# Optimization experiments

Measured on AMD Instinct MI355X. Metric: run time of the kernel, lower is better.

The kernel has to match this reference:

```python
import jax, jax.numpy as jnp
import numpy as np

B, S, D, H, HD, NF, NL, V = 16, 2048, 768, 12, 64, 32, 12, 2362
EPS = 1e-6  # fast_transformers LinearAttention eps


def _rope_tables(seq_len, dim):
    inv_freq = 1.0 / (10000.0 ** (jnp.arange(0, dim, 2, dtype=jnp.float32) / dim))
    t = jnp.arange(seq_len, dtype=jnp.float32)
    freqs = jnp.einsum('s,f->sf', t, inv_freq)
    emb = jnp.concatenate([freqs, freqs], axis=-1)[None, :, None, :]  # [1,S,1,HD]
    return jnp.cos(emb), jnp.sin(emb)


def _rot_half(x):
    x1, x2 = jnp.split(x, 2, axis=-1)
    return jnp.concatenate([-x2, x1], axis=-1)


def _ln(x, g, b):
    m = jnp.mean(x, axis=-1, keepdims=True)
    v = jnp.var(x, axis=-1, keepdims=True)
    return (x - m) / jnp.sqrt(v + 1e-5) * g + b


def setup_inputs():
    key = jax.random.key(0)
    ks = jax.random.split(key, 16)
    w = lambda k, shape: jax.random.normal(k, shape, jnp.float32) * 0.02
    return {
        'idx': jax.random.randint(ks[0], (B, S), 0, V),
        'mask': jnp.ones((B, S), jnp.int32),
        'emb': w(ks[1], (V, D)),
        'wq': w(ks[2], (NL, D, D)), 'bq': jnp.zeros((NL, D), jnp.float32),
        'wk': w(ks[3], (NL, D, D)), 'bk': jnp.zeros((NL, D), jnp.float32),
        'wv': w(ks[4], (NL, D, D)), 'bv': jnp.zeros((NL, D), jnp.float32),
        'wo': w(ks[5], (NL, D, D)), 'bo': jnp.zeros((NL, D), jnp.float32),
        'omega': jax.random.normal(ks[6], (NL, HD, NF), jnp.float32),
        'g1': jnp.ones((NL, D), jnp.float32), 'be1': jnp.zeros((NL, D), jnp.float32),
        'w1': w(ks[7], (NL, D, D)), 'c1': jnp.zeros((NL, D), jnp.float32),
        'w2': w(ks[8], (NL, D, D)), 'c2': jnp.zeros((NL, D), jnp.float32),
        'g2': jnp.ones((NL, D), jnp.float32), 'be2': jnp.zeros((NL, D), jnp.float32),
        'gf': jnp.ones((D,), jnp.float32), 'bf': jnp.zeros((D,), jnp.float32),
    }


def reference(idx, mask, emb, wq, bq, wk, bk, wv, bv, wo, bo, omega,
              g1, be1, w1, c1, w2, c2, g2, be2, gf, bf):
    x = emb[idx]                     # token embedding [B,S,D]; dropout = identity (eval)
    m = mask.astype(x.dtype)         # LengthMask from mask.sum(-1); mask is contiguous ones
    cos, sin = _rope_tables(S, HD)
    for l in range(NL):
        q = (x @ wq[l] + bq[l]).reshape(B, S, H, HD)
        k = (x @ wk[l] + bk[l]).reshape(B, S, H, HD)
        v = (x @ wv[l] + bv[l]).reshape(B, S, H, HD)
        q = q * cos + _rot_half(q) * sin
        k = k * cos + _rot_half(k) * sin
        # GeneralizedRandomFeatures: phi(x) = relu(x @ omega)
        Qf = jax.nn.relu(jnp.einsum('bshd,df->bshf', q, omega[l]))
        Kf = jax.nn.relu(jnp.einsum('bshd,df->bshf', k, omega[l])) * m[:, :, None, None]
        KV = jnp.einsum('bshf,bshd->bhfd', Kf, v)                       # [B,H,NF,HD]
        Z = 1.0 / (jnp.einsum('bshf,bhf->bsh', Qf, Kf.sum(axis=1)) + EPS)
        a = jnp.einsum('bshf,bhfd,bsh->bshd', Qf, KV, Z).reshape(B, S, D)
        x = x + (a @ wo[l] + bo[l])           # residual (dropout=identity)
        x = _ln(x, g1[l], be1[l])             # post-norm
        y = jax.nn.gelu(x @ w1[l] + c1[l], approximate=False) @ w2[l] + c2[l]
        x = _ln(x + y, g2[l], be2[l])
    return _ln(x, gf, bf)                     # final encoder LayerNorm
```

## Files before the change

kernel.cpp:

```cpp
#include <hip/hip_runtime.h>
#include <cstdint>
#include <cstddef>

typedef __bf16 bf16;
typedef __bf16 bf16x8 __attribute__((ext_vector_type(8)));
typedef __bf16 bf16x4 __attribute__((ext_vector_type(4)));
typedef float f32x4 __attribute__((ext_vector_type(4)));

#define NB 16
#define SS 2048
#define HH 12
#define NLL 12
#define MTOK (NB*SS)

#define BARRIER() do { asm volatile("" ::: "memory"); __builtin_amdgcn_s_barrier(); asm volatile("" ::: "memory"); } while (0)
#define VMCNT0()  asm volatile("s_waitcnt vmcnt(0)" ::: "memory")
#define SCHEDB()  __builtin_amdgcn_sched_barrier(0)

__device__ __forceinline__ void load16_lds(const bf16* g, bf16* l) {
    __builtin_amdgcn_global_load_lds((const __attribute__((address_space(1))) void*)g,
                                     (__attribute__((address_space(3))) void*)l, 16, 0, 0);
}

__global__ void diag_k(float* out, float code) {
    if (threadIdx.x == 0 && blockIdx.x == 0) out[0] = code;
}

__global__ __launch_bounds__(256) void packw_k(const float* __restrict__ wq, const float* __restrict__ wk,
                                               const float* __restrict__ wv, const float* __restrict__ wo,
                                               const float* __restrict__ w1, const float* __restrict__ w2,
                                               int l, bf16* qkvT_l, bf16* oT_l, bf16* w1T_l, bf16* w2T_l) {
    __shared__ float tile[32][33];
    int which = blockIdx.z;
    const float* srcs[6] = {wq, wk, wv, wo, w1, w2};
    const float* src = srcs[which] + (size_t)l * 589824;
    bf16* dst;
    if (which < 3)       dst = qkvT_l + (size_t)which * 589824;
    else if (which == 3) dst = oT_l;
    else if (which == 4) dst = w1T_l;
    else                 dst = w2T_l;
    int tx = threadIdx.x, ty = threadIdx.y;
    int bx = blockIdx.x, by = blockIdx.y;
#pragma unroll
    for (int j = 0; j < 4; ++j)
        tile[ty + j*8][tx] = src[(size_t)(by*32 + ty + j*8) * 768 + bx*32 + tx];
    __syncthreads();
#pragma unroll
    for (int j = 0; j < 4; ++j)
        dst[(size_t)(bx*32 + ty + j*8) * 768 + by*32 + tx] = (bf16)tile[tx][ty + j*8];
}

__global__ void packb_k(const float* __restrict__ bq, const float* __restrict__ bk,
                        const float* __restrict__ bv, float* bqkv) {
    int i = blockIdx.x * 256 + threadIdx.x;
    if (i >= NLL * 2304) return;
    int l = i / 2304, c = i % 2304;
    float v = (c < 768) ? bq[l*768 + c] : (c < 1536) ? bk[l*768 + c - 768] : bv[l*768 + c - 1536];
    bqkv[i] = v;
}

__global__ void rope_k(float* cosT, float* sinT) {
    int i = blockIdx.x * 256 + threadIdx.x;
    int s = i >> 6, j = i & 63, f = j & 31;
    float inv = powf(10000.f, -(float)(2*f) * (1.0f/64.0f));
    float ang = (float)s * inv;
    cosT[i] = cosf(ang);
    sinT[i] = sinf(ang);
}

__global__ __launch_bounds__(192) void embed_k(const int* __restrict__ idx, const float* __restrict__ emb,
                                               float* __restrict__ x, bf16* __restrict__ xb) {
    size_t tok = blockIdx.x;
    int t = threadIdx.x;
    int id = idx[tok];
    float4 v = *(const float4*)&emb[(size_t)id * 768 + t*4];
    *(float4*)&x[tok * 768 + t*4] = v;
    bf16x4 o; o[0] = (bf16)v.x; o[1] = (bf16)v.y; o[2] = (bf16)v.z; o[3] = (bf16)v.w;
    *(bf16x4*)&xb[tok * 768 + t*4] = o;
}

__global__ __launch_bounds__(512, 2)
void gemm256_k(const bf16* __restrict__ A, const bf16* __restrict__ Bt,
               const float* __restrict__ bias, bf16* __restrict__ outb, int N) {
    const int K = 768;
    __shared__ bf16 As[2][16384];
    __shared__ bf16 Bs[2][16384];
    const int t = threadIdx.x;
    const int w = t >> 6, lane = t & 63;
    const int wr = w >> 2, wc = w & 3;

    const int nx = gridDim.x;
    const int L = blockIdx.y * nx + blockIdx.x;
    const int xcd = L & 7, bi = L >> 3;
    const int bcol = (bi % nx) * 256;
    const int brow = ((bi / nx) * 8 + xcd) * 256;

    const int srow0 = t >> 3;
    const int scb   = (t & 7) * 16;
    const int scbs  = scb ^ ((srow0 & 7) << 4);
    const int scol  = scbs >> 1;

    auto stageA = [&](int s, int k0, int hh) {
        const bf16* g0 = A + (size_t)(brow + hh*128 + srow0)      * K + k0 + scol;
        const bf16* g1 = A + (size_t)(brow + hh*128 + srow0 + 64) * K + k0 + scol;
        load16_lds(g0, &As[s][hh*8192 + t*8]);
        load16_lds(g1, &As[s][hh*8192 + t*8 + 4096]);
    };
    auto stageB = [&](int s, int k0, int hh) {
        const bf16* g0 = Bt + (size_t)(bcol + hh*128 + srow0)      * K + k0 + scol;
        const bf16* g1 = Bt + (size_t)(bcol + hh*128 + srow0 + 64) * K + k0 + scol;
        load16_lds(g0, &Bs[s][hh*8192 + t*8]);
        load16_lds(g1, &Bs[s][hh*8192 + t*8 + 4096]);
    };

    const int rowa = lane & 15, kg = lane >> 4;
    const int rsw  = (rowa & 7) << 4;

    f32x4  acc[8][4] = {};
    bf16x8 af[4][2];
    bf16x8 bg[2][2][2];

#define LOADAF(CUR, MH)                                                          \
    _Pragma("unroll") for (int mi2 = 0; mi2 < 4; ++mi2)                          \
    _Pragma("unroll") for (int ks = 0; ks < 2; ++ks) {                           \
        int lrow = wr*128 + (MH)*64 + mi2*16 + rowa;                             \
        int cbyt = (ks*64 + kg*16) ^ rsw;                                        \
        af[mi2][ks] = *(const bf16x8*)&As[CUR][lrow*64 + (cbyt >> 1)];           \
    }
#define LOADBG(CUR, NH)                                                          \
    _Pragma("unroll") for (int ni2 = 0; ni2 < 2; ++ni2)                          \
    _Pragma("unroll") for (int ks = 0; ks < 2; ++ks) {                           \
        int lrow = wc*64 + (NH)*32 + ni2*16 + rowa;                              \
        int cbyt = (ks*64 + kg*16) ^ rsw;                                        \
        bg[NH][ni2][ks] = *(const bf16x8*)&Bs[CUR][lrow*64 + (cbyt >> 1)];       \
    }
#define MFMAQ(MH, NH)                                                            \
    __builtin_amdgcn_s_setprio(1);                                               \
    _Pragma("unroll") for (int mi2 = 0; mi2 < 4; ++mi2)                          \
    _Pragma("unroll") for (int ni2 = 0; ni2 < 2; ++ni2)                          \
    _Pragma("unroll") for (int ks = 0; ks < 2; ++ks)                             \
        acc[(MH)*4+mi2][(NH)*2+ni2] = __builtin_amdgcn_mfma_f32_16x16x32_bf16(   \
            af[mi2][ks], bg[NH][ni2][ks], acc[(MH)*4+mi2][(NH)*2+ni2], 0, 0, 0); \
    __builtin_amdgcn_s_setprio(0);

    stageA(0, 0, 0); stageA(0, 0, 1); stageB(0, 0, 0); stageB(0, 0, 1);
    VMCNT0();
    BARRIER();

    for (int kt = 0; kt < 12; ++kt) {
        const int cur = kt & 1, nb = cur ^ 1;
        const int kn = (kt + 1) * 64;
        const bool st = (kt < 11);
        if (st) { stageA(nb, kn, 0); stageA(nb, kn, 1); stageB(nb, kn, 0); stageB(nb, kn, 1); }
        LOADAF(cur, 0);
        LOADBG(cur, 0);
        MFMAQ(0, 0);
        SCHEDB();
        LOADBG(cur, 1);
        MFMAQ(0, 1);
        SCHEDB();
        LOADAF(cur, 1);
        MFMAQ(1, 1);
        SCHEDB();
        MFMAQ(1, 0);
        VMCNT0();
        BARRIER();
    }
#undef LOADAF
#undef LOADBG
#undef MFMAQ

    bf16* Cs = &As[0][0];
    const int r0 = (lane >> 4) * 4, c0 = lane & 15;
    const int ch = t & 15, rr = t >> 4;
#pragma unroll
    for (int h = 0; h < 2; ++h) {
        __syncthreads();
        if ((wc >> 1) == h) {
            const int lc0 = (wc & 1) * 64;
#pragma unroll
            for (int mi = 0; mi < 8; ++mi)
#pragma unroll
                for (int ni = 0; ni < 4; ++ni) {
                    int col = bcol + wc * 64 + ni * 16 + c0;
                    float bv = bias[col];
#pragma unroll
                    for (int r = 0; r < 4; ++r)
                        Cs[(wr*128 + mi*16 + r0 + r) * 128 + lc0 + ni*16 + c0] =
                            (bf16)(acc[mi][ni][r] + bv);
                }
        }
        __syncthreads();
#pragma unroll
        for (int i = 0; i < 8; ++i) {
            int row = rr + i * 32;
            *(bf16x8*)&outb[(size_t)(brow + row) * N + bcol + h*128 + ch*8] =
                *(const bf16x8*)&Cs[row * 128 + ch * 8];
        }
    }
}

template <int MODE>
__global__ __launch_bounds__(256)
void gemm128_k(const bf16* __restrict__ A, const bf16* __restrict__ Bt,
               const float* __restrict__ bias, bf16* __restrict__ outb, int N) {
    const int K = 768;
    __shared__ bf16 sh[16384];
    bf16* As = sh;
    bf16* Bs = sh + 8192;
    const int t = threadIdx.x;
    const int w = t >> 6, lane = t & 63;
    const int wr = w >> 1, wc = w & 1;

    const int nx = gridDim.x;
    const int L = blockIdx.y * nx + blockIdx.x;
    const int xcd = L & 7, bi = L >> 3;
    const int bcol = (bi % nx) * 128;
    const int brow = ((bi / nx) * 8 + xcd) * 128;

    const int srow = t >> 3;
    const int scol = (((t & 7) * 16) ^ ((srow & 7) << 4)) >> 1;
    const int rowa = lane & 15, kg = lane >> 4;
    const int rsw  = (rowa & 7) << 4;

    f32x4 acc[4][4] = {};

    for (int k0 = 0; k0 < K; k0 += 64) {
        __syncthreads();
#pragma unroll
        for (int j = 0; j < 4; ++j) {
            load16_lds(A  + (size_t)(brow + j*32 + srow) * K + k0 + scol, &As[j*2048 + t*8]);
            load16_lds(Bt + (size_t)(bcol + j*32 + srow) * K + k0 + scol, &Bs[j*2048 + t*8]);
        }
        __syncthreads();
        bf16x8 af[4][2], bg[4][2];
#pragma unroll
        for (int mi = 0; mi < 4; ++mi)
#pragma unroll
            for (int ks = 0; ks < 2; ++ks)
                af[mi][ks] = *(const bf16x8*)&As[(wr*64 + mi*16 + rowa)*64 + (((ks*64 + kg*16) ^ rsw) >> 1)];
#pragma unroll
        for (int ni = 0; ni < 4; ++ni)
#pragma unroll
            for (int ks = 0; ks < 2; ++ks)
                bg[ni][ks] = *(const bf16x8*)&Bs[(wc*64 + ni*16 + rowa)*64 + (((ks*64 + kg*16) ^ rsw) >> 1)];
#pragma unroll
        for (int mi = 0; mi < 4; ++mi)
#pragma unroll
            for (int ni = 0; ni < 4; ++ni)
#pragma unroll
                for (int ks = 0; ks < 2; ++ks)
                    acc[mi][ni] = __builtin_amdgcn_mfma_f32_16x16x32_bf16(af[mi][ks], bg[ni][ks], acc[mi][ni], 0, 0, 0);
    }

    __syncthreads();
    const int r0 = (lane >> 4) * 4, c0 = lane & 15;
#pragma unroll
    for (int mi = 0; mi < 4; ++mi)
#pragma unroll
        for (int ni = 0; ni < 4; ++ni) {
            int col = bcol + wc * 64 + ni * 16 + c0;
            float bv = bias[col];
#pragma unroll
            for (int r = 0; r < 4; ++r) {
                float v = acc[mi][ni][r] + bv;
                if (MODE == 1) v = 0.5f * v * (1.f + erff(v * 0.70710678118f));
                sh[(wr*64 + mi*16 + r0 + r) * 128 + wc*64 + ni*16 + c0] = (bf16)v;
            }
        }
    __syncthreads();
    const int ch = t & 15, rr = t >> 4;
#pragma unroll
    for (int i = 0; i < 8; ++i) {
        int row = rr + i * 16;
        *(bf16x8*)&outb[(size_t)(brow + row) * N + bcol + ch*8] =
            *(const bf16x8*)&sh[row * 128 + ch * 8];
    }
}

__global__ __launch_bounds__(192) void phi_k(const bf16* __restrict__ qkv, const float* __restrict__ cosT,
                                             const float* __restrict__ sinT, const float* __restrict__ omega_l,
                                             const int* __restrict__ mask, bf16* __restrict__ Qf,
                                             bf16* __restrict__ Kf) {
    __shared__ float roped[2][4][12][65];
    __shared__ float om[64][32];
    int t = threadIdx.x;
    size_t tok0 = (size_t)blockIdx.x * 4;

    for (int i = t; i < 2048; i += 192) ((float*)om)[i] = omega_l[i];

    {
        int side = t / 96, cr = t % 96, h = cr >> 3, cq = cr & 7;
        float sgn = (cq < 4) ? -1.f : 1.f;
        for (int it = 0; it < 4; ++it) {
            size_t tokg = tok0 + it;
            int s = (int)(tokg & (SS - 1));
            const bf16* rowp = qkv + tokg * 2304 + side * 768 + h * 64;
            bf16x8 mv = *(const bf16x8*)(rowp + cq * 8);
            bf16x8 pv = *(const bf16x8*)(rowp + (cq ^ 4) * 8);
            const float* cp = cosT + s * 64 + cq * 8;
            const float* sp = sinT + s * 64 + cq * 8;
#pragma unroll
            for (int e = 0; e < 8; ++e) {
                float r = (float)mv[e] * cp[e] + sgn * (float)pv[e] * sp[e];
                roped[side][it][h][cq * 8 + e] = r;
            }
        }
    }
    __syncthreads();

    int side = t / 96, rr = t % 96, h = rr >> 3, f0 = (rr & 7) * 4;
    float acc[4][4] = {};
    for (int d = 0; d < 64; ++d) {
        float4 o = *(const float4*)&om[d][f0];
#pragma unroll
        for (int tk = 0; tk < 4; ++tk) {
            float qv = roped[side][tk][h][d];
            acc[tk][0] += qv * o.x; acc[tk][1] += qv * o.y;
            acc[tk][2] += qv * o.z; acc[tk][3] += qv * o.w;
        }
    }
    bf16* outb = (side == 0) ? Qf : Kf;
#pragma unroll
    for (int tk = 0; tk < 4; ++tk) {
        size_t tokg = tok0 + tk;
        float m = (side == 1) ? (float)mask[tokg] : 1.f;
        bf16x4 v;
        v[0] = (bf16)(fmaxf(acc[tk][0], 0.f) * m);
        v[1] = (bf16)(fmaxf(acc[tk][1], 0.f) * m);
        v[2] = (bf16)(fmaxf(acc[tk][2], 0.f) * m);
        v[3] = (bf16)(fmaxf(acc[tk][3], 0.f) * m);
        *(bf16x4*)&outb[(tokg * 12 + h) * 32 + f0] = v;
    }
}

__global__ __launch_bounds__(256) void kvp_k(const bf16* __restrict__ Kf, const bf16* __restrict__ qkv,
                                             float* __restrict__ KVp, float* __restrict__ Ksp) {
    int ch = blockIdx.x, h = blockIdx.y, b = blockIdx.z;
    __shared__ float kts[64][32];
    __shared__ bf16 vts[64][64];
    int t = threadIdx.x;
    int fg = t & 15, dg = t >> 4;
    int f0 = fg * 2, d0 = dg * 4;
    float acc[8] = {};
    float ksm[2] = {};
    for (int s0 = ch * 256; s0 < ch * 256 + 256; s0 += 64) {
        __syncthreads();
        {
            int row = t >> 2, slot = t & 3;
            bf16x8 k8 = *(const bf16x8*)&Kf[((size_t)(b * SS + s0 + row) * 12 + h) * 32 + slot * 8];
#pragma unroll
            for (int e = 0; e < 8; ++e) kts[row][slot * 8 + e] = (float)k8[e];
            int c0 = t, c1 = t + 256;
            *(float4*)&vts[c0 >> 3][(c0 & 7) * 8] =
                *(const float4*)&qkv[(size_t)(b * SS + s0 + (c0 >> 3)) * 2304 + 1536 + h * 64 + (c0 & 7) * 8];
            *(float4*)&vts[c1 >> 3][(c1 & 7) * 8] =
                *(const float4*)&qkv[(size_t)(b * SS + s0 + (c1 >> 3)) * 2304 + 1536 + h * 64 + (c1 & 7) * 8];
        }
        __syncthreads();
#pragma unroll 4
        for (int sl = 0; sl < 64; ++sl) {
            float2 kk = *(const float2*)&kts[sl][f0];
            bf16x4 vv = *(const bf16x4*)&vts[sl][d0];
            float v0 = (float)vv[0], v1 = (float)vv[1], v2 = (float)vv[2], v3 = (float)vv[3];
            acc[0] += kk.x * v0; acc[1] += kk.x * v1; acc[2] += kk.x * v2; acc[3] += kk.x * v3;
            acc[4] += kk.y * v0; acc[5] += kk.y * v1; acc[6] += kk.y * v2; acc[7] += kk.y * v3;
            if (dg == 0) { ksm[0] += kk.x; ksm[1] += kk.y; }
        }
    }
    size_t base = (((size_t)(b * 12 + h) * 8 + ch) * 32) * 64;
#pragma unroll
    for (int i = 0; i < 2; ++i)
#pragma unroll
        for (int j = 0; j < 4; ++j)
            KVp[base + (size_t)(f0 + i) * 64 + d0 + j] = acc[i * 4 + j];
    if (dg == 0) {
        size_t kb = ((size_t)(b * 12 + h) * 8 + ch) * 32;
        Ksp[kb + f0] = ksm[0]; Ksp[kb + f0 + 1] = ksm[1];
    }
}

__global__ __launch_bounds__(256) void kvc_k(const float* __restrict__ KVp, const float* __restrict__ Ksp,
                                             float* __restrict__ KV, float* __restrict__ Ksum) {
    int bh = blockIdx.x, t = threadIdx.x;
    size_t base = (size_t)bh * 8 * 2048;
    float v[8] = {};
    for (int ch = 0; ch < 8; ++ch)
#pragma unroll
        for (int j = 0; j < 8; ++j) v[j] += KVp[base + (size_t)ch * 2048 + t * 8 + j];
#pragma unroll
    for (int j = 0; j < 8; ++j) KV[(size_t)bh * 2048 + t * 8 + j] = v[j];
    if (t < 32) {
        float s = 0.f;
        for (int ch = 0; ch < 8; ++ch) s += Ksp[((size_t)bh * 8 + ch) * 32 + t];
        Ksum[(size_t)bh * 32 + t] = s;
    }
}

__global__ __launch_bounds__(256) void comb_k(const bf16* __restrict__ Qf, const float* __restrict__ KV,
                                              const float* __restrict__ Ksum, bf16* __restrict__ aout) {
    int ch = blockIdx.x, h = blockIdx.y, b = blockIdx.z;
    int bh = b * 12 + h;
    int t = threadIdx.x, sl = t >> 6, d = t & 63;
    const float* kvb = KV + (size_t)bh * 2048;
    const float* ksb = Ksum + (size_t)bh * 32;
    float kvcol[32], ksr[32];
#pragma unroll
    for (int f = 0; f < 32; ++f) kvcol[f] = kvb[f * 64 + d];
#pragma unroll
    for (int f = 0; f < 32; ++f) ksr[f] = ksb[f];
    for (int g = 0; g < 16; ++g) {
        int s = ch * 64 + g * 4 + sl;
        size_t tok = (size_t)b * SS + s;
        const bf16* qf = Qf + (tok * 12 + h) * 32;
        float accd = 0.f, accz = 0.f;
#pragma unroll
        for (int fb = 0; fb < 4; ++fb) {
            bf16x8 q8 = *(const bf16x8*)(qf + fb * 8);
#pragma unroll
            for (int e = 0; e < 8; ++e) {
                float q = (float)q8[e];
                accd += q * kvcol[fb * 8 + e];
                accz += q * ksr[fb * 8 + e];
            }
        }
        float z = 1.f / (accz + 1e-6f);
        aout[tok * 768 + h * 64 + d] = (bf16)(accd * z);
    }
}

__global__ __launch_bounds__(192) void ln2_k(const float* xsrc, const bf16* ysrc,
                                             const float* __restrict__ g, const float* __restrict__ be,
                                             float* xout, bf16* xbout) {
    size_t tok = blockIdx.x;
    int t = threadIdx.x;
    float4 v = *(const float4*)&xsrc[tok * 768 + t * 4];
    if (ysrc) {
        bf16x4 yv = *(const bf16x4*)&ysrc[tok * 768 + t * 4];
        v.x += (float)yv[0]; v.y += (float)yv[1]; v.z += (float)yv[2]; v.w += (float)yv[3];
    }
    float s = v.x + v.y + v.z + v.w;
    float q = v.x * v.x + v.y * v.y + v.z * v.z + v.w * v.w;
#pragma unroll
    for (int off = 32; off > 0; off >>= 1) { s += __shfl_down(s, off); q += __shfl_down(q, off); }
    __shared__ float sred[3], qred[3];
    int w = t >> 6, lane = t & 63;
    if (lane == 0) { sred[w] = s; qred[w] = q; }
    __syncthreads();
    s = sred[0] + sred[1] + sred[2];
    q = qred[0] + qred[1] + qred[2];
    float mean = s * (1.f / 768.f);
    float var = q * (1.f / 768.f) - mean * mean;
    float inv = rsqrtf(var + 1e-5f);
    float4 gg = *(const float4*)&g[t * 4];
    float4 bb = *(const float4*)&be[t * 4];
    float4 o;
    o.x = (v.x - mean) * inv * gg.x + bb.x;
    o.y = (v.y - mean) * inv * gg.y + bb.y;
    o.z = (v.z - mean) * inv * gg.z + bb.z;
    o.w = (v.w - mean) * inv * gg.w + bb.w;
    *(float4*)&xout[tok * 768 + t * 4] = o;
    if (xbout) {
        bf16x4 ob; ob[0] = (bf16)o.x; ob[1] = (bf16)o.y; ob[2] = (bf16)o.z; ob[3] = (bf16)o.w;
        *(bf16x4*)&xbout[tok * 768 + t * 4] = ob;
    }
}

extern "C" void kernel_launch(void* const* d_in, const int* in_sizes, int n_in,
                              void* d_out, int out_size, void* d_ws, size_t ws_size,
                              hipStream_t stream) {
    const int*   idx   = (const int*)d_in[0];
    const int*   mask  = (const int*)d_in[1];
    const float* emb   = (const float*)d_in[2];
    const float* wq    = (const float*)d_in[3];
    const float* bq    = (const float*)d_in[4];
    const float* wk    = (const float*)d_in[5];
    const float* bk    = (const float*)d_in[6];
    const float* wv    = (const float*)d_in[7];
    const float* bv    = (const float*)d_in[8];
    const float* wo    = (const float*)d_in[9];
    const float* bo    = (const float*)d_in[10];
    const float* omega = (const float*)d_in[11];
    const float* g1    = (const float*)d_in[12];
    const float* be1   = (const float*)d_in[13];
    const float* w1    = (const float*)d_in[14];
    const float* c1    = (const float*)d_in[15];
    const float* w2    = (const float*)d_in[16];
    const float* c2    = (const float*)d_in[17];
    const float* g2    = (const float*)d_in[18];
    const float* be2   = (const float*)d_in[19];
    const float* gf    = (const float*)d_in[20];
    const float* bff   = (const float*)d_in[21];
    float* dout = (float*)d_out;

    char* wsb = (char*)d_ws;
    size_t off = 0;
    auto nxt = [&](size_t bytes) -> void* {
        void* p = wsb + off;
        off += bytes;
        off = (off + 255) & ~(size_t)255;
        return p;
    };

    float* cosT  = (float*)nxt((size_t)SS * 64 * 4);
    float* sinT  = (float*)nxt((size_t)SS * 64 * 4);
    bf16*  qkvTl = (bf16*)nxt((size_t)2304 * 768 * 2);
    bf16*  oTl   = (bf16*)nxt((size_t)768 * 768 * 2);
    bf16*  w1Tl  = (bf16*)nxt((size_t)768 * 768 * 2);
    bf16*  w2Tl  = (bf16*)nxt((size_t)768 * 768 * 2);
    float* bqkv  = (float*)nxt((size_t)NLL * 2304 * 4);
    float* x     = (float*)nxt((size_t)MTOK * 768 * 4);
    bf16*  xb    = (bf16*)nxt((size_t)MTOK * 768 * 2);
    bf16*  qkv   = (bf16*)nxt((size_t)MTOK * 2304 * 2);
    bf16*  Qf    = (bf16*)nxt((size_t)MTOK * 384 * 2);
    bf16*  Kf    = (bf16*)nxt((size_t)MTOK * 384 * 2);
    float* KVp   = (float*)nxt((size_t)NB * HH * 8 * 2048 * 4);
    float* Ksp   = (float*)nxt((size_t)NB * HH * 8 * 32 * 4);
    float* KV    = (float*)nxt((size_t)NB * HH * 2048 * 4);
    float* Ksum  = (float*)nxt((size_t)NB * HH * 32 * 4);
    size_t needed = off;

    if (ws_size < needed) {
        diag_k<<<dim3(1), dim3(64), 0, stream>>>(dout, 10000.f + (float)(ws_size >> 20));
        return;
    }

    bf16* abuf = qkv;
    bf16* h1   = (bf16*)((char*)qkv + (size_t)MTOK * 768 * 2);
    bf16* y    = (bf16*)((char*)qkv + (size_t)MTOK * 768 * 4);

    packb_k<<<dim3((NLL * 2304 + 255) / 256), dim3(256), 0, stream>>>(bq, bk, bv, bqkv);
    rope_k<<<dim3(SS * 64 / 256), dim3(256), 0, stream>>>(cosT, sinT);
    embed_k<<<dim3(MTOK), dim3(192), 0, stream>>>(idx, emb, x, xb);

    for (int l = 0; l < NLL; ++l) {
        const float* bqkv_l = bqkv + (size_t)l * 2304;
        const float* om_l   = omega + (size_t)l * 2048;

        packw_k<<<dim3(24, 24, 6), dim3(32, 8), 0, stream>>>(wq, wk, wv, wo, w1, w2, l, qkvTl, oTl, w1Tl, w2Tl);
        gemm256_k<<<dim3(9, 128), dim3(512), 0, stream>>>(xb, qkvTl, bqkv_l, qkv, 2304);
        phi_k<<<dim3(MTOK / 4), dim3(192), 0, stream>>>(qkv, cosT, sinT, om_l, mask, Qf, Kf);
        kvp_k<<<dim3(8, HH, NB), dim3(256), 0, stream>>>(Kf, qkv, KVp, Ksp);
        kvc_k<<<dim3(NB * HH), dim3(256), 0, stream>>>(KVp, Ksp, KV, Ksum);
        comb_k<<<dim3(32, HH, NB), dim3(256), 0, stream>>>(Qf, KV, Ksum, abuf);
        gemm128_k<0><<<dim3(6, 256), dim3(256), 0, stream>>>(abuf, oTl, bo + (size_t)l * 768, y, 768);
        ln2_k<<<dim3(MTOK), dim3(192), 0, stream>>>(x, y, g1 + (size_t)l * 768, be1 + (size_t)l * 768, x, xb);
        gemm128_k<1><<<dim3(6, 256), dim3(256), 0, stream>>>(xb, w1Tl, c1 + (size_t)l * 768, h1, 768);
        gemm128_k<0><<<dim3(6, 256), dim3(256), 0, stream>>>(h1, w2Tl, c2 + (size_t)l * 768, y, 768);
        ln2_k<<<dim3(MTOK), dim3(192), 0, stream>>>(x, y, g2 + (size_t)l * 768, be2 + (size_t)l * 768, x,
                                                    (l == NLL - 1) ? nullptr : xb);
    }
    ln2_k<<<dim3(MTOK), dim3(192), 0, stream>>>(x, nullptr, gf, bff, dout, nullptr);
}
```

Measured before the change: 7.458 ms.

## Retile QKV GEMM to 256x128 blocks with BK=32 for higher occupancy

Replaces the 256x256 QKV projection GEMM (BK=64, 8 waves in a 2x4 grid, interleaved fragment loads and MFMA phases) with a 256x128 tile at BK=32 and a 4x2 wave grid. The goal is to shrink shared memory from 128KB to 48KB so four blocks can share a CU, and to double the grid so the work spreads over more blocks. The main loop is simpler: all fragments are loaded, the next stage is issued, then a barrier and a 4x4 MFMA burst, with a second barrier each iteration. In exchange, each byte of A loaded gets less reuse, and there are twice as many K iterations and barriers.

After: 7.312 ms. Within noise of the previous version (-2.0%).

```diff
diff --git a/kernel.cpp b/kernel.cpp
--- a/kernel.cpp
+++ b/kernel.cpp
@@ -15,7 +15,6 @@
 
 #define BARRIER() do { asm volatile("" ::: "memory"); __builtin_amdgcn_s_barrier(); asm volatile("" ::: "memory"); } while (0)
 #define VMCNT0()  asm volatile("s_waitcnt vmcnt(0)" ::: "memory")
-#define SCHEDB()  __builtin_amdgcn_sched_barrier(0)
 
 __device__ __forceinline__ void load16_lds(const bf16* g, bf16* l) {
     __builtin_amdgcn_global_load_lds((const __attribute__((address_space(1))) void*)g,
@@ -79,123 +78,90 @@
     *(bf16x4*)&xb[tok * 768 + t*4] = o;
 }
 
-__global__ __launch_bounds__(512, 2)
-void gemm256_k(const bf16* __restrict__ A, const bf16* __restrict__ Bt,
+__global__ __launch_bounds__(512, 4)
+void gemmqkv_k(const bf16* __restrict__ A, const bf16* __restrict__ Bt,
                const float* __restrict__ bias, bf16* __restrict__ outb, int N) {
     const int K = 768;
-    __shared__ bf16 As[2][16384];
-    __shared__ bf16 Bs[2][16384];
+    __shared__ bf16 sh[24576];
     const int t = threadIdx.x;
     const int w = t >> 6, lane = t & 63;
-    const int wr = w >> 2, wc = w & 3;
+    const int wr = w >> 1, wc = w & 1;
 
     const int nx = gridDim.x;
     const int L = blockIdx.y * nx + blockIdx.x;
     const int xcd = L & 7, bi = L >> 3;
-    const int bcol = (bi % nx) * 256;
+    const int bcol = (bi % nx) * 128;
     const int brow = ((bi / nx) * 8 + xcd) * 256;
 
-    const int srow0 = t >> 3;
-    const int scb   = (t & 7) * 16;
-    const int scbs  = scb ^ ((srow0 & 7) << 4);
-    const int scol  = scbs >> 1;
-
-    auto stageA = [&](int s, int k0, int hh) {
-        const bf16* g0 = A + (size_t)(brow + hh*128 + srow0)      * K + k0 + scol;
-        const bf16* g1 = A + (size_t)(brow + hh*128 + srow0 + 64) * K + k0 + scol;
-        load16_lds(g0, &As[s][hh*8192 + t*8]);
-        load16_lds(g1, &As[s][hh*8192 + t*8 + 4096]);
+    const int srow = t >> 2;
+    const int scol = (((t & 3) * 16) ^ ((srow & 3) << 4)) >> 1;
+
+    auto stageA = [&](int s, int k0) {
+        load16_lds(A + (size_t)(brow + srow)       * K + k0 + scol, &sh[s*8192 + t*8]);
+        load16_lds(A + (size_t)(brow + 128 + srow) * K + k0 + scol, &sh[s*8192 + 4096 + t*8]);
     };
-    auto stageB = [&](int s, int k0, int hh) {
-        const bf16* g0 = Bt + (size_t)(bcol + hh*128 + srow0)      * K + k0 + scol;
-        const bf16* g1 = Bt + (size_t)(bcol + hh*128 + srow0 + 64) * K + k0 + scol;
-        load16_lds(g0, &Bs[s][hh*8192 + t*8]);
-        load16_lds(g1, &Bs[s][hh*8192 + t*8 + 4096]);
+    auto stageB = [&](int s, int k0) {
+        load16_lds(Bt + (size_t)(bcol + srow)      * K + k0 + scol, &sh[16384 + s*4096 + t*8]);
     };
 
     const int rowa = lane & 15, kg = lane >> 4;
-    const int rsw  = (rowa & 7) << 4;
-
-    f32x4  acc[8][4] = {};
-    bf16x8 af[4][2];
-    bf16x8 bg[2][2][2];
-
-#define LOADAF(CUR, MH)                                                          \
-    _Pragma("unroll") for (int mi2 = 0; mi2 < 4; ++mi2)                          \
-    _Pragma("unroll") for (int ks = 0; ks < 2; ++ks) {                           \
-        int lrow = wr*128 + (MH)*64 + mi2*16 + rowa;                             \
-        int cbyt = (ks*64 + kg*16) ^ rsw;                                        \
-        af[mi2][ks] = *(const bf16x8*)&As[CUR][lrow*64 + (cbyt >> 1)];           \
-    }
-#define LOADBG(CUR, NH)                                                          \
-    _Pragma("unroll") for (int ni2 = 0; ni2 < 2; ++ni2)                          \
-    _Pragma("unroll") for (int ks = 0; ks < 2; ++ks) {                           \
-        int lrow = wc*64 + (NH)*32 + ni2*16 + rowa;                              \
-        int cbyt = (ks*64 + kg*16) ^ rsw;                                        \
-        bg[NH][ni2][ks] = *(const bf16x8*)&Bs[CUR][lrow*64 + (cbyt >> 1)];       \
-    }
-#define MFMAQ(MH, NH)                                                            \
-    __builtin_amdgcn_s_setprio(1);                                               \
-    _Pragma("unroll") for (int mi2 = 0; mi2 < 4; ++mi2)                          \
-    _Pragma("unroll") for (int ni2 = 0; ni2 < 2; ++ni2)                          \
-    _Pragma("unroll") for (int ks = 0; ks < 2; ++ks)                             \
-        acc[(MH)*4+mi2][(NH)*2+ni2] = __builtin_amdgcn_mfma_f32_16x16x32_bf16(   \
-            af[mi2][ks], bg[NH][ni2][ks], acc[(MH)*4+mi2][(NH)*2+ni2], 0, 0, 0); \
-    __builtin_amdgcn_s_setprio(0);
-
-    stageA(0, 0, 0); stageA(0, 0, 1); stageB(0, 0, 0); stageB(0, 0, 1);
+    const int celem = ((kg * 16) ^ ((rowa & 3) << 4)) >> 1;
+
+    f32x4  acc[4][4] = {};
+    bf16x8 af[4], bg[4];
+
+    stageA(0, 0); stageB(0, 0);
     VMCNT0();
     BARRIER();
 
-    for (int kt = 0; kt < 12; ++kt) {
+    for (int kt = 0; kt < 24; ++kt) {
         const int cur = kt & 1, nb = cur ^ 1;
-        const int kn = (kt + 1) * 64;
-        const bool st = (kt < 11);
-        if (st) { stageA(nb, kn, 0); stageA(nb, kn, 1); stageB(nb, kn, 0); stageB(nb, kn, 1); }
-        LOADAF(cur, 0);
-        LOADBG(cur, 0);
-        MFMAQ(0, 0);
-        SCHEDB();
-        LOADBG(cur, 1);
-        MFMAQ(0, 1);
-        SCHEDB();
-        LOADAF(cur, 1);
-        MFMAQ(1, 1);
-        SCHEDB();
-        MFMAQ(1, 0);
+        const int kn = (kt + 1) * 32;
+        const bool st = (kt < 23);
+#pragma unroll
+        for (int mi = 0; mi < 4; ++mi)
+            af[mi] = *(const bf16x8*)&sh[cur*8192 + (wr*64 + mi*16 + rowa)*32 + celem];
+#pragma unroll
+        for (int ni = 0; ni < 4; ++ni)
+            bg[ni] = *(const bf16x8*)&sh[16384 + cur*4096 + (wc*64 + ni*16 + rowa)*32 + celem];
+        if (st) { stageA(nb, kn); stageB(nb, kn); }
+        BARRIER();
+        __builtin_amdgcn_s_setprio(1);
+#pragma unroll
+        for (int mi = 0; mi < 4; ++mi)
+#pragma unroll
+            for (int ni = 0; ni < 4; ++ni)
+                acc[mi][ni] = __builtin_amdgcn_mfma_f32_16x16x32_bf16(af[mi], bg[ni], acc[mi][ni], 0, 0, 0);
+        __builtin_amdgcn_s_setprio(0);
         VMCNT0();
         BARRIER();
     }
-#undef LOADAF
-#undef LOADBG
-#undef MFMAQ
-
-    bf16* Cs = &As[0][0];
+
+    bf16* Cs = sh;
     const int r0 = (lane >> 4) * 4, c0 = lane & 15;
-    const int ch = t & 15, rr = t >> 4;
+    const int ch = t & 7, rr = t >> 3;
 #pragma unroll
     for (int h = 0; h < 2; ++h) {
         __syncthreads();
-        if ((wc >> 1) == h) {
-            const int lc0 = (wc & 1) * 64;
-#pragma unroll
-            for (int mi = 0; mi < 8; ++mi)
+        if (wc == h) {
+#pragma unroll
+            for (int mi = 0; mi < 4; ++mi)
 #pragma unroll
                 for (int ni = 0; ni < 4; ++ni) {
                     int col = bcol + wc * 64 + ni * 16 + c0;
                     float bv = bias[col];
 #pragma unroll
                     for (int r = 0; r < 4; ++r)
-                        Cs[(wr*128 + mi*16 + r0 + r) * 128 + lc0 + ni*16 + c0] =
+                        Cs[(wr*64 + mi*16 + r0 + r) * 64 + ni*16 + c0] =
                             (bf16)(acc[mi][ni][r] + bv);
                 }
         }
         __syncthreads();
 #pragma unroll
-        for (int i = 0; i < 8; ++i) {
-            int row = rr + i * 32;
-            *(bf16x8*)&outb[(size_t)(brow + row) * N + bcol + h*128 + ch*8] =
-                *(const bf16x8*)&Cs[row * 128 + ch * 8];
+        for (int i = 0; i < 4; ++i) {
+            int row = rr + i * 64;
+            *(bf16x8*)&outb[(size_t)(brow + row) * N + bcol + h*64 + ch*8] =
+                *(const bf16x8*)&Cs[row * 64 + ch * 8];
         }
     }
 }
@@ -538,7 +504,7 @@
         const float* om_l   = omega + (size_t)l * 2048;
 
         packw_k<<<dim3(24, 24, 6), dim3(32, 8), 0, stream>>>(wq, wk, wv, wo, w1, w2, l, qkvTl, oTl, w1Tl, w2Tl);
-        gemm256_k<<<dim3(9, 128), dim3(512), 0, stream>>>(xb, qkvTl, bqkv_l, qkv, 2304);
+        gemmqkv_k<<<dim3(18, 128), dim3(512), 0, stream>>>(xb, qkvTl, bqkv_l, qkv, 2304);
         phi_k<<<dim3(MTOK / 4), dim3(192), 0, stream>>>(qkv, cosT, sinT, om_l, mask, Qf, Kf);
         kvp_k<<<dim3(8, HH, NB), dim3(256), 0, stream>>>(Kf, qkv, KVp, Ksp);
         kvc_k<<<dim3(NB * HH), dim3(256), 0, stream>>>(KVp, Ksp, KV, Ksum);
```
